# Kernel tuning notes

Measured on AMD Instinct MI355X. Metric: run time of the kernel, lower is better.

Reference implementation:

```python
import jax, jax.numpy as jnp
import numpy as np

HID = 128      # hidden_dim
CDIM = 128     # c_dim
NBLK = 5       # n_blocks
RESO = 32      # grid_resolution
G = RESO ** 3  # number of voxels
B, T = 2, 100000


def setup_inputs() -> dict:
    key = jax.random.key(0)
    ks = jax.random.split(key, 8)
    return {
        "points": jax.random.normal(ks[0], (B, T, 3), jnp.float32),
        "index": jax.random.randint(ks[1], (B, 1, T), 0, G, dtype=jnp.int64),
        # fc_pos: Linear(3, 2*HID)
        "fc_pos_w": jax.random.normal(ks[2], (3, 2 * HID), jnp.float32) * 0.1,
        "fc_pos_b": jnp.zeros((2 * HID,), jnp.float32),
        # ResnetBlockFC(2*HID, HID) x NBLK: fc_0 (2H->H), fc_1 (H->H), shortcut (2H->H, no bias)
        "fc0_w": jax.random.normal(ks[3], (NBLK, 2 * HID, HID), jnp.float32) * 0.05,
        "fc0_b": jnp.zeros((NBLK, HID), jnp.float32),
        "fc1_w": jax.random.normal(ks[4], (NBLK, HID, HID), jnp.float32) * 0.05,
        "fc1_b": jnp.zeros((NBLK, HID), jnp.float32),
        "sc_w": jax.random.normal(ks[5], (NBLK, 2 * HID, HID), jnp.float32) * 0.05,
        # fc_c: Linear(HID, CDIM)
        "fc_c_w": jax.random.normal(ks[6], (HID, CDIM), jnp.float32) * 0.05,
        "fc_c_b": jnp.zeros((CDIM,), jnp.float32),
    }


def _resnet_block(x, w0, b0, w1, b1, ws):
    # ResnetBlockFC: net = fc_0(relu(x)); dx = fc_1(relu(net)); out = shortcut(x) + dx
    net = jnp.maximum(x, 0.0) @ w0 + b0
    dx = jnp.maximum(net, 0.0) @ w1 + b1
    return x @ ws + dx


def reference(points, index, fc_pos_w, fc_pos_b, fc0_w, fc0_b, fc1_w, fc1_b, sc_w, fc_c_w, fc_c_b):
    idx = index[:, 0, :]  # [B, T]

    def pool_local(net):
        # scatter_max over voxels, then gather back per point
        seg = jax.vmap(lambda c_b, i_b: jax.ops.segment_max(c_b, i_b, num_segments=G))(net, idx)  # [B,G,H]
        return jnp.take_along_axis(seg, idx[:, :, None], axis=1)  # [B,T,H]; every gathered voxel is non-empty

    net = points @ fc_pos_w + fc_pos_b          # [B,T,2H]
    net = _resnet_block(net, fc0_w[0], fc0_b[0], fc1_w[0], fc1_b[0], sc_w[0])  # [B,T,H]
    for i in range(1, NBLK):
        pooled = pool_local(net)
        net = jnp.concatenate([net, pooled], axis=2)  # [B,T,2H]
        net = _resnet_block(net, fc0_w[i], fc0_b[i], fc1_w[i], fc1_b[i], sc_w[i])

    c = net @ fc_c_w + fc_c_b  # [B,T,CDIM]

    # generate_grid_features: scatter_mean into the 32^3 grid (zeros for empty voxels)
    sums = jax.vmap(lambda c_b, i_b: jax.ops.segment_sum(c_b, i_b, num_segments=G))(c, idx)  # [B,G,CDIM]
    cnts = jax.vmap(lambda i_b: jax.ops.segment_sum(jnp.ones((T,), c.dtype), i_b, num_segments=G))(idx)  # [B,G]
    cnts = cnts[:, :, None]
    mean = jnp.where(cnts > 0, sums / jnp.maximum(cnts, 1.0), 0.0)
    fea_grid = jnp.transpose(mean, (0, 2, 1)).reshape(B, CDIM, RESO, RESO, RESO)
    return fea_grid
```

## Files before the change

kernel.cpp:

```cpp
#include <hip/hip_runtime.h>

#define T_PTS 100000
#define NB 2
#define NROWS (NB * T_PTS)
#define GCELLS 32768
#define NCELL (NB * GCELLS)
#define HID 128
#define MBLK 64
#define GRID_RB (NROWS / MBLK)

typedef __attribute__((ext_vector_type(8))) short bf16x8;
typedef __attribute__((ext_vector_type(4))) float f32x4;

#define MFMA16 __builtin_amdgcn_mfma_f32_16x16x32_bf16

__device__ __forceinline__ unsigned short bf16rne(float f) {
  unsigned u = __float_as_uint(f);
  return (unsigned short)((u + 0x7FFFu + ((u >> 16) & 1u)) >> 16);
}
__device__ __forceinline__ void bf16split(float f, unsigned short& h,
                                          unsigned short& l) {
  h = bf16rne(f);
  l = bf16rne(f - __uint_as_float(((unsigned)h) << 16));
}
__device__ __forceinline__ unsigned packhl(float f) {
  unsigned short h, l;
  bf16split(f, h, l);
  return (((unsigned)h) << 16) | (unsigned)l;
}

union U8 { bf16x8 v; unsigned u[4]; };

__device__ __forceinline__ void up2(unsigned w0, unsigned w1, unsigned& h,
                                    unsigned& l) {
  h = __builtin_amdgcn_perm(w1, w0, 0x07060302u);
  l = __builtin_amdgcn_perm(w1, w0, 0x05040100u);
}

__device__ __forceinline__ void relu2(unsigned qh, unsigned ql, unsigned& rh,
                                      unsigned& rl) {
  const unsigned keep = ((~qh >> 15) & 0x00010001u) * 0xFFFFu;
  rh = qh & keep;
  rl = ql & keep;
}

__device__ __forceinline__ void dma16(const unsigned* g, unsigned* l) {
  __builtin_amdgcn_global_load_lds(
      (const __attribute__((address_space(1))) unsigned*)g,
      (__attribute__((address_space(3))) unsigned*)l, 16, 0, 0);
}

template <int MODE>
__global__ __launch_bounds__(256, 4) void resblock_mfma(
    const void* __restrict__ srcv, const float* __restrict__ posw,
    const float* __restrict__ posb, const unsigned* __restrict__ cell,
    const int* __restrict__ perm, const int* __restrict__ vcell,
    const unsigned short* __restrict__ w0p, const float* __restrict__ b0,
    const unsigned short* __restrict__ w1p, const float* __restrict__ b1,
    const unsigned short* __restrict__ swp, unsigned* __restrict__ net_out) {
  __shared__ unsigned lds32[8192];
  const int tid = threadIdx.x;
  const int lane = tid & 63;
  const int wid = tid >> 6;
  const int wc = wid;
  const int t0 = blockIdx.x * MBLK;

  const int srow = wid * 16 + (lane & 15);
  const int skc4 = (lane >> 4) * 4;
  const long vrow = (long)t0 + srow;
  const unsigned* nrowL = nullptr;
  const unsigned* crowL = nullptr;
  float pp0 = 0.f, pp1 = 0.f, pp2 = 0.f;
  if (MODE == 1) {
    nrowL = (const unsigned*)srcv + vrow * HID;
    crowL = cell + (long)vcell[vrow] * HID;
  } else {
    const float* ppp = (const float*)srcv + (long)perm[vrow] * 3;
    pp0 = ppp[0]; pp1 = ppp[1]; pp2 = ppp[2];
  }

  auto stage_dma = [&](int ks) {
    unsigned* base = &lds32[((ks & 1) << 11) + wid * 256];
    const unsigned* rowp = (ks < 4) ? nrowL : crowL;
    const int ko = ((ks & 3) << 4) + skc4;
    dma16(rowp + ko, base);
    dma16(rowp + 64 + ko, base + 1024);
  };
  auto stage0 = [&](int ks) {
    const int kb = ks * 32 + (lane >> 4) * 8;
    float xv[8];
#pragma unroll
    for (int i = 0; i < 8; i += 4) {
      float4 wa = *(const float4*)(posw + kb + i);
      float4 wb = *(const float4*)(posw + 256 + kb + i);
      float4 wcc = *(const float4*)(posw + 512 + kb + i);
      float4 bb = *(const float4*)(posb + kb + i);
      xv[i + 0] = fmaf(pp0, wa.x, fmaf(pp1, wb.x, fmaf(pp2, wcc.x, bb.x)));
      xv[i + 1] = fmaf(pp0, wa.y, fmaf(pp1, wb.y, fmaf(pp2, wcc.y, bb.y)));
      xv[i + 2] = fmaf(pp0, wa.z, fmaf(pp1, wb.z, fmaf(pp2, wcc.z, bb.z)));
      xv[i + 3] = fmaf(pp0, wa.w, fmaf(pp1, wb.w, fmaf(pp2, wcc.w, bb.w)));
    }
    unsigned ph[8];
#pragma unroll
    for (int i = 0; i < 8; ++i) ph[i] = packhl(xv[i]);
    uint4 xh4, xl4;
    up2(ph[0], ph[1], xh4.x, xl4.x);
    up2(ph[2], ph[3], xh4.y, xl4.y);
    up2(ph[4], ph[5], xh4.z, xl4.z);
    up2(ph[6], ph[7], xh4.w, xl4.w);
    const int db = ((ks & 1) << 11) + wid * 256 + lane * 4;
    *(uint4*)&lds32[db] = xh4;
    *(uint4*)&lds32[db + 1024] = xl4;
  };
  auto load_B = [&](const unsigned short* base, int loOff, int ks, bf16x8* h,
                    bf16x8* l) {
#pragma unroll
    for (int nt = 0; nt < 2; ++nt) {
      const int fi = (ks * 8 + wc * 2 + nt) * 512 + lane * 8;
      h[nt] = *(const bf16x8*)(base + fi);
      l[nt] = *(const bf16x8*)(base + loOff + fi);
    }
  };

  f32x4 accy[4][2], acco[4][2];
#pragma unroll
  for (int i = 0; i < 4; ++i)
#pragma unroll
    for (int j = 0; j < 2; ++j) {
      f32x4 z = {0.f, 0.f, 0.f, 0.f};
      accy[i][j] = z;
      acco[i][j] = z;
    }

  bf16x8 b1h[2], b1l[2], b2h[2], b2l[2];
  if (MODE == 1) {
    stage_dma(0);
  } else {
    stage0(0);
  }
  load_B(w0p, 32768, 0, b1h, b1l);
  __syncthreads();

#pragma unroll 1
  for (int ks = 0; ks < 8; ++ks) {
    const int sb = (ks & 1) << 11;
    load_B(swp, 32768, ks, b2h, b2l);
    if (MODE == 1 && ks < 7) stage_dma(ks + 1);
    __builtin_amdgcn_s_setprio(1);
#pragma unroll
    for (int mt = 0; mt < 4; ++mt) {
      const unsigned* px = &lds32[sb + mt * 256 + lane * 4];
      U8 xh, xl, rh, rl;
      xh.v = *(const bf16x8*)px;
      xl.v = *(const bf16x8*)(px + 1024);
#pragma unroll
      for (int i = 0; i < 4; ++i) relu2(xh.u[i], xl.u[i], rh.u[i], rl.u[i]);
#pragma unroll
      for (int nt = 0; nt < 2; ++nt) {
        accy[mt][nt] = MFMA16(rh.v, b1h[nt], accy[mt][nt], 0, 0, 0);
        accy[mt][nt] = MFMA16(rh.v, b1l[nt], accy[mt][nt], 0, 0, 0);
        accy[mt][nt] = MFMA16(rl.v, b1h[nt], accy[mt][nt], 0, 0, 0);
      }
    }
    __builtin_amdgcn_s_setprio(0);
    asm volatile("" ::: "memory");
    if (ks < 7) load_B(w0p, 32768, ks + 1, b1h, b1l);
    __builtin_amdgcn_s_setprio(1);
#pragma unroll
    for (int mt = 0; mt < 4; ++mt) {
      const unsigned* px = &lds32[sb + mt * 256 + lane * 4];
      bf16x8 xh = *(const bf16x8*)px;
      bf16x8 xl = *(const bf16x8*)(px + 1024);
#pragma unroll
      for (int nt = 0; nt < 2; ++nt) {
        acco[mt][nt] = MFMA16(xh, b2h[nt], acco[mt][nt], 0, 0, 0);
        acco[mt][nt] = MFMA16(xh, b2l[nt], acco[mt][nt], 0, 0, 0);
        acco[mt][nt] = MFMA16(xl, b2h[nt], acco[mt][nt], 0, 0, 0);
      }
    }
    __builtin_amdgcn_s_setprio(0);
    if (MODE == 0 && ks < 7) stage0(ks + 1);
    __syncthreads();
  }

  {
    float b0v[2];
#pragma unroll
    for (int nt = 0; nt < 2; ++nt)
      b0v[nt] = b0[wc * 32 + nt * 16 + (lane & 15)];
#pragma unroll
    for (int mt = 0; mt < 4; ++mt) {
#pragma unroll
      for (int nt = 0; nt < 2; ++nt) {
        const int c = wc * 32 + nt * 16 + (lane & 15);
        const int k2 = c >> 5;
        const int j = c & 7;
        const int lahi = ((c & 31) >> 3) * 16;
#pragma unroll
        for (int r = 0; r < 4; ++r) {
          float h = fmaxf(accy[mt][nt][r] + b0v[nt], 0.f);
          int la = lahi + (lane >> 4) * 4 + r;
          la ^= (la >> 3) & 7;
          lds32[((k2 * 4 + mt) * 64 + la) * 8 + j] = packhl(h);
        }
      }
    }
  }
  __syncthreads();

  {
    const int lar2 = lane ^ ((lane >> 3) & 7);
#pragma unroll
    for (int k2 = 0; k2 < 4; ++k2) {
      bf16x8 ch[2], cl[2];
      load_B(w1p, 16384, k2, ch, cl);
      __builtin_amdgcn_s_setprio(1);
#pragma unroll
      for (int mt = 0; mt < 4; ++mt) {
        const unsigned* p = &lds32[((k2 * 4 + mt) * 64 + lar2) * 8];
        uint4 q1 = *(const uint4*)p;
        uint4 q2 = *(const uint4*)(p + 4);
        unsigned q[8] = {q1.x, q1.y, q1.z, q1.w, q2.x, q2.y, q2.z, q2.w};
        U8 ah, al;
#pragma unroll
        for (int p2 = 0; p2 < 4; ++p2)
          up2(q[2 * p2], q[2 * p2 + 1], ah.u[p2], al.u[p2]);
#pragma unroll
        for (int nt = 0; nt < 2; ++nt) {
          acco[mt][nt] = MFMA16(ah.v, ch[nt], acco[mt][nt], 0, 0, 0);
          acco[mt][nt] = MFMA16(ah.v, cl[nt], acco[mt][nt], 0, 0, 0);
          acco[mt][nt] = MFMA16(al.v, ch[nt], acco[mt][nt], 0, 0, 0);
        }
      }
      __builtin_amdgcn_s_setprio(0);
    }
  }

  {
    float b1v[2];
#pragma unroll
    for (int nt = 0; nt < 2; ++nt)
      b1v[nt] = b1[wc * 32 + nt * 16 + (lane & 15)];
#pragma unroll
    for (int mt = 0; mt < 4; ++mt) {
#pragma unroll
      for (int r = 0; r < 4; ++r) {
        const int row = mt * 16 + (lane >> 4) * 4 + r;
        unsigned short* op =
            (unsigned short*)(net_out + ((long)t0 + row) * HID);
        unsigned short h, l;
        bf16split(acco[mt][0][r] + b1v[0], h, l);
        op[wc * 32 + (lane & 15)] = h;
        op[128 + wc * 32 + (lane & 15)] = l;
        bf16split(acco[mt][1][r] + b1v[1], h, l);
        op[wc * 32 + 16 + (lane & 15)] = h;
        op[128 + wc * 32 + 16 + (lane & 15)] = l;
      }
    }
  }
}

__global__ __launch_bounds__(256, 4) void final_mfma(
    unsigned* __restrict__ net, const unsigned short* __restrict__ wcp,
    const float* __restrict__ bc) {
  __shared__ unsigned lds32[4096];
  const int tid = threadIdx.x;
  const int lane = tid & 63;
  const int wid = tid >> 6;
  const int wc = wid;
  const int t0 = blockIdx.x * MBLK;

  const int srow = wid * 16 + (lane & 15);
  const int skc4 = (lane >> 4) * 4;
  const unsigned* nrowL = net + ((long)t0 + srow) * HID;

  auto stage = [&](int ks) {
    unsigned* base = &lds32[((ks & 1) << 11) + wid * 256];
    const int ko = (ks << 4) + skc4;
    dma16(nrowL + ko, base);
    dma16(nrowL + 64 + ko, base + 1024);
  };
  auto load_B = [&](int ks, bf16x8* h, bf16x8* l) {
#pragma unroll
    for (int nt = 0; nt < 2; ++nt) {
      const int fi = (ks * 8 + wc * 2 + nt) * 512 + lane * 8;
      h[nt] = *(const bf16x8*)(wcp + fi);
      l[nt] = *(const bf16x8*)(wcp + 16384 + fi);
    }
  };

  f32x4 acc[4][2];
#pragma unroll
  for (int i = 0; i < 4; ++i)
#pragma unroll
    for (int j = 0; j < 2; ++j) {
      f32x4 z = {0.f, 0.f, 0.f, 0.f};
      acc[i][j] = z;
    }

  bf16x8 ch[2], cl[2];
  stage(0);
  load_B(0, ch, cl);
  __syncthreads();

#pragma unroll 1
  for (int ks = 0; ks < 4; ++ks) {
    const int sb = (ks & 1) << 11;
    if (ks < 3) stage(ks + 1);
    __builtin_amdgcn_s_setprio(1);
#pragma unroll
    for (int mt = 0; mt < 2; ++mt) {
      const unsigned* px = &lds32[sb + mt * 256 + lane * 4];
      bf16x8 xh = *(const bf16x8*)px;
      bf16x8 xl = *(const bf16x8*)(px + 1024);
#pragma unroll
      for (int nt = 0; nt < 2; ++nt) {
        acc[mt][nt] = MFMA16(xh, ch[nt], acc[mt][nt], 0, 0, 0);
        acc[mt][nt] = MFMA16(xh, cl[nt], acc[mt][nt], 0, 0, 0);
        acc[mt][nt] = MFMA16(xl, ch[nt], acc[mt][nt], 0, 0, 0);
      }
    }
    __builtin_amdgcn_s_setprio(0);
    bf16x8 sh[2], sl[2];
#pragma unroll
    for (int nt = 0; nt < 2; ++nt) { sh[nt] = ch[nt]; sl[nt] = cl[nt]; }
    if (ks < 3) load_B(ks + 1, ch, cl);
    __builtin_amdgcn_s_setprio(1);
#pragma unroll
    for (int mt = 2; mt < 4; ++mt) {
      const unsigned* px = &lds32[sb + mt * 256 + lane * 4];
      bf16x8 xh = *(const bf16x8*)px;
      bf16x8 xl = *(const bf16x8*)(px + 1024);
#pragma unroll
      for (int nt = 0; nt < 2; ++nt) {
        acc[mt][nt] = MFMA16(xh, sh[nt], acc[mt][nt], 0, 0, 0);
        acc[mt][nt] = MFMA16(xh, sl[nt], acc[mt][nt], 0, 0, 0);
        acc[mt][nt] = MFMA16(xl, sh[nt], acc[mt][nt], 0, 0, 0);
      }
    }
    __builtin_amdgcn_s_setprio(0);
    __syncthreads();
  }

  float* fout = (float*)net;
  float bcv[2];
#pragma unroll
  for (int nt = 0; nt < 2; ++nt)
    bcv[nt] = bc[wc * 32 + nt * 16 + (lane & 15)];
#pragma unroll
  for (int mt = 0; mt < 4; ++mt) {
#pragma unroll
    for (int r = 0; r < 4; ++r) {
      const int row = mt * 16 + (lane >> 4) * 4 + r;
      float* op = fout + ((long)t0 + row) * HID;
      op[wc * 32 + (lane & 15)] = acc[mt][0][r] + bcv[0];
      op[wc * 32 + 16 + (lane & 15)] = acc[mt][1][r] + bcv[1];
    }
  }
}

__global__ void pack_weights(const float* __restrict__ fc0,
                             const float* __restrict__ fc1,
                             const float* __restrict__ sc,
                             const float* __restrict__ fcc,
                             unsigned short* __restrict__ w0p,
                             unsigned short* __restrict__ w1p,
                             unsigned short* __restrict__ swp,
                             unsigned short* __restrict__ wcp) {
  int gid = blockIdx.x * 256 + threadIdx.x;
  const float* src;
  unsigned short* dst;
  int K, e;
  if (gid < 163840) { src = fc0; dst = w0p; K = 256; e = gid; }
  else if (gid < 327680) { src = sc; dst = swp; K = 256; e = gid - 163840; }
  else if (gid < 409600) { src = fc1; dst = w1p; K = 128; e = gid - 327680; }
  else if (gid < 425984) { src = fcc; dst = wcp; K = 128; e = gid - 409600; }
  else return;
  const int mat = e / (K * 128);
  const int r = e - mat * K * 128;
  const int k = r >> 7, n = r & 127;
  const float x = src[e];
  unsigned short hi, lo;
  bf16split(x, hi, lo);
  const int ks = k >> 5, lg = (k >> 3) & 3, j = k & 7;
  const int l = lg * 16 + (n & 15), nt = n >> 4;
  unsigned short* mb = dst + (long)mat * K * 256;
  const int off = ((ks * 8 + nt) * 64 + l) * 8 + j;
  mb[off] = hi;
  mb[off + K * 128] = lo;
}

__global__ void zero_i32(int* __restrict__ p, int n) {
  const int i = blockIdx.x * 256 + threadIdx.x;
  if (i < n) p[i] = 0;
}

__global__ void count_csr(const int* __restrict__ idx, int* __restrict__ curs) {
  const int gid = blockIdx.x * 256 + threadIdx.x;
  if (gid >= NROWS) return;
  const int b = gid / T_PTS;
  atomicAdd(&curs[b * GCELLS + idx[gid]], 1);
}

__global__ __launch_bounds__(1024) void scan_csr(const int* __restrict__ cnt,
                                                 int* __restrict__ offsets) {
  __shared__ int part[1024];
  const int t = threadIdx.x;
  const int base = t * (NCELL / 1024);
  int s = 0;
  for (int i = 0; i < NCELL / 1024; ++i) s += cnt[base + i];
  part[t] = s;
  __syncthreads();
  for (int d = 1; d < 1024; d <<= 1) {
    int v = (t >= d) ? part[t - d] : 0;
    __syncthreads();
    part[t] += v;
    __syncthreads();
  }
  int run = (t == 0) ? 0 : part[t - 1];
  for (int i = 0; i < NCELL / 1024; ++i) {
    offsets[base + i] = run;
    run += cnt[base + i];
  }
  if (t == 1023) offsets[NCELL] = run;
}

__global__ void scatter_csr(const int* __restrict__ idx,
                            const int* __restrict__ offsets,
                            int* __restrict__ curs, int* __restrict__ perm,
                            int* __restrict__ vcell) {
  const int gid = blockIdx.x * 256 + threadIdx.x;
  if (gid >= NROWS) return;
  const int b = gid / T_PTS;
  const int cellk = b * GCELLS + idx[gid];
  const int slot = offsets[cellk] + atomicAdd(&curs[cellk], 1);
  perm[slot] = gid;
  vcell[slot] = cellk;
}

__global__ __launch_bounds__(256) void pool_csr(const unsigned* __restrict__ net,
                                                const int* __restrict__ offsets,
                                                unsigned* __restrict__ cellf) {
  const int cellk = blockIdx.x * 4 + (threadIdx.x >> 6);
  const int lane = threadIdx.x & 63;
  const int s0 = offsets[cellk], s1 = offsets[cellk + 1];
  if (s0 >= s1) return;
  float m0 = -3.402823466e38f, m1 = -3.402823466e38f;
  unsigned h0 = 0u, l0 = 0u, h1 = 0u, l1 = 0u;
  for (int row = s0; row < s1; ++row) {
    const unsigned* rp = net + (long)row * HID;
    unsigned hi = rp[lane];
    unsigned lo = rp[64 + lane];
    float v0 = __uint_as_float(hi << 16) + __uint_as_float(lo << 16);
    float v1 = __uint_as_float(hi & 0xFFFF0000u) +
               __uint_as_float(lo & 0xFFFF0000u);
    if (v0 > m0) { m0 = v0; h0 = hi; l0 = lo; }
    if (v1 > m1) { m1 = v1; h1 = hi; l1 = lo; }
  }
  unsigned* cp = cellf + (long)cellk * HID;
  cp[lane] = (h0 & 0xFFFFu) | (h1 & 0xFFFF0000u);
  cp[64 + lane] = (l0 & 0xFFFFu) | (l1 & 0xFFFF0000u);
}

__global__ __launch_bounds__(256) void cellsum_mean(
    const float* __restrict__ c, const int* __restrict__ offsets,
    float* __restrict__ out) {
  __shared__ float ts[64][129];
  __shared__ float cf[64];
  const int t = threadIdx.x;
  const int b = blockIdx.x >> 9;
  const int g0 = (blockIdx.x & 511) * 64;
  const int cell0 = b * GCELLS + g0;
  {
    const int ci = t >> 2;
    const int c0 = (t & 3) * 32;
    const int s0 = offsets[cell0 + ci], s1 = offsets[cell0 + ci + 1];
    float acc[32];
#pragma unroll
    for (int j = 0; j < 32; ++j) acc[j] = 0.f;
    for (int row = s0; row < s1; ++row) {
      const float* rp = c + (long)row * HID + c0;
#pragma unroll
      for (int j = 0; j < 32; j += 4) {
        float4 v = *(const float4*)(rp + j);
        acc[j + 0] += v.x;
        acc[j + 1] += v.y;
        acc[j + 2] += v.z;
        acc[j + 3] += v.w;
      }
    }
#pragma unroll
    for (int j = 0; j < 32; ++j) ts[ci][c0 + j] = acc[j];
    if ((t & 3) == 0) cf[ci] = (float)(s1 - s0);
  }
  __syncthreads();
  const int lane = t & 63;
  const int w = t >> 6;
  float* ob = out + (long)b * HID * GCELLS + g0 + lane;
  const float cnt = cf[lane];
  const bool nz = cnt > 0.f;
  const float inv = nz ? 1.0f / cnt : 0.f;
#pragma unroll 4
  for (int cc = w; cc < HID; cc += 4) {
    float v = ts[lane][cc] * inv;
    ob[(long)cc * GCELLS] = nz ? v : 0.f;
  }
}

extern "C" void kernel_launch(void* const* d_in, const int* in_sizes, int n_in,
                              void* d_out, int out_size, void* d_ws,
                              size_t ws_size, hipStream_t stream) {
  const float* points = (const float*)d_in[0];
  const int* idx = (const int*)d_in[1];
  const float* fc_pos_w = (const float*)d_in[2];
  const float* fc_pos_b = (const float*)d_in[3];
  const float* fc0_w = (const float*)d_in[4];
  const float* fc0_b = (const float*)d_in[5];
  const float* fc1_w = (const float*)d_in[6];
  const float* fc1_b = (const float*)d_in[7];
  const float* sc_w = (const float*)d_in[8];
  const float* fc_c_w = (const float*)d_in[9];
  const float* fc_c_b = (const float*)d_in[10];
  float* out = (float*)d_out;

  const long NET_BYTES = (long)NROWS * HID * 4;
  const long CELL_BYTES = (long)NCELL * HID * 4;
  unsigned* net = (unsigned*)d_ws;
  unsigned* cellf = (unsigned*)((char*)d_ws + NET_BYTES);
  int* offsets = (int*)((char*)d_ws + NET_BYTES + CELL_BYTES);

  unsigned short* packs = (unsigned short*)d_out;
  unsigned short* w0p = packs;
  unsigned short* swp = packs + 327680;
  unsigned short* w1p = packs + 655360;
  unsigned short* wcp = packs + 819200;
  int* curs = (int*)((char*)d_out + (2l << 20));
  int* perm = (int*)((char*)d_out + (3l << 20));
  int* vcell = (int*)((char*)d_out + (4l << 20));

  const int GRID_PTS = (NROWS + 255) / 256;
  const int GRID_ZERO = (NCELL + 255) / 256;
  const int GRID_CELL = NCELL / 4;
  const int GRID_CM = NCELL / 64;

  pack_weights<<<1664, 256, 0, stream>>>(fc0_w, fc1_w, sc_w, fc_c_w, w0p, w1p,
                                         swp, wcp);

  zero_i32<<<GRID_ZERO, 256, 0, stream>>>(curs, NCELL);
  count_csr<<<GRID_PTS, 256, 0, stream>>>(idx, curs);
  scan_csr<<<1, 1024, 0, stream>>>(curs, offsets);
  zero_i32<<<GRID_ZERO, 256, 0, stream>>>(curs, NCELL);
  scatter_csr<<<GRID_PTS, 256, 0, stream>>>(idx, offsets, curs, perm, vcell);

  resblock_mfma<0><<<GRID_RB, 256, 0, stream>>>(
      points, fc_pos_w, fc_pos_b, nullptr, perm, vcell, w0p, fc0_b, w1p,
      fc1_b, swp, net);

  for (int i = 1; i < 5; ++i) {
    pool_csr<<<GRID_CELL, 256, 0, stream>>>(net, offsets, cellf);
    resblock_mfma<1><<<GRID_RB, 256, 0, stream>>>(
        net, nullptr, nullptr, cellf, perm, vcell, w0p + (long)i * 65536,
        fc0_b + i * HID, w1p + (long)i * 32768, fc1_b + i * HID,
        swp + (long)i * 65536, net);
  }

  final_mfma<<<GRID_RB, 256, 0, stream>>>(net, wcp, fc_c_b);
  cellsum_mean<<<GRID_CM, 256, 0, stream>>>((const float*)net, offsets, out);
}
```

Measured before the change: 721.9 us.

## Switch resnet and final GEMMs from 16x16x32 to 32x32x16 bf16 MFMA

Replaces the 16x16x32 bf16 MFMA tiling with 32x32x16 MFMA in the resnet block and final linear kernels. Each wave now owns two 32x32 output tiles instead of eight 16x16 tiles. The packed weight layout, the LDS layout for the intermediate activation and the epilogue row/column mapping are all rewritten to match. The larger MFMA shape needs fewer instructions and fewer B-fragment loads per FLOP. In exchange it uses larger accumulators and changes the LDS access patterns, which could cause bank conflicts in the new hidden-activation store layout.

```diff
diff --git a/kernel.cpp b/kernel.cpp
--- a/kernel.cpp
+++ b/kernel.cpp
@@ -10,9 +10,9 @@
 #define GRID_RB (NROWS / MBLK)
 
 typedef __attribute__((ext_vector_type(8))) short bf16x8;
-typedef __attribute__((ext_vector_type(4))) float f32x4;
-
-#define MFMA16 __builtin_amdgcn_mfma_f32_16x16x32_bf16
+typedef __attribute__((ext_vector_type(16))) float f32x16;
+
+#define MFMA32 __builtin_amdgcn_mfma_f32_32x32x16_bf16
 
 __device__ __forceinline__ unsigned short bf16rne(float f) {
   unsigned u = __float_as_uint(f);
@@ -115,22 +115,19 @@
   auto load_B = [&](const unsigned short* base, int loOff, int ks, bf16x8* h,
                     bf16x8* l) {
 #pragma unroll
-    for (int nt = 0; nt < 2; ++nt) {
-      const int fi = (ks * 8 + wc * 2 + nt) * 512 + lane * 8;
-      h[nt] = *(const bf16x8*)(base + fi);
-      l[nt] = *(const bf16x8*)(base + loOff + fi);
+    for (int kh = 0; kh < 2; ++kh) {
+      const int fi = ((ks * 2 + kh) * 4 + wc) * 512 + lane * 8;
+      h[kh] = *(const bf16x8*)(base + fi);
+      l[kh] = *(const bf16x8*)(base + loOff + fi);
     }
   };
 
-  f32x4 accy[4][2], acco[4][2];
-#pragma unroll
-  for (int i = 0; i < 4; ++i)
-#pragma unroll
-    for (int j = 0; j < 2; ++j) {
-      f32x4 z = {0.f, 0.f, 0.f, 0.f};
-      accy[i][j] = z;
-      acco[i][j] = z;
-    }
+  f32x16 accy[2], acco[2];
+#pragma unroll
+  for (int i = 0; i < 2; ++i) {
+#pragma unroll
+    for (int j = 0; j < 16; ++j) { accy[i][j] = 0.f; acco[i][j] = 0.f; }
+  }
 
   bf16x8 b1h[2], b1l[2], b2h[2], b2l[2];
   if (MODE == 1) {
@@ -140,6 +137,10 @@
   }
   load_B(w0p, 32768, 0, b1h, b1l);
   __syncthreads();
+
+  const int amt0 = (lane >> 4) & 1;
+  const int akq0 = lane >> 5;
+  const int ari = lane & 15;
 
 #pragma unroll 1
   for (int ks = 0; ks < 8; ++ks) {
@@ -148,18 +149,19 @@
     if (MODE == 1 && ks < 7) stage_dma(ks + 1);
     __builtin_amdgcn_s_setprio(1);
 #pragma unroll
-    for (int mt = 0; mt < 4; ++mt) {
-      const unsigned* px = &lds32[sb + mt * 256 + lane * 4];
-      U8 xh, xl, rh, rl;
-      xh.v = *(const bf16x8*)px;
-      xl.v = *(const bf16x8*)(px + 1024);
-#pragma unroll
-      for (int i = 0; i < 4; ++i) relu2(xh.u[i], xl.u[i], rh.u[i], rl.u[i]);
-#pragma unroll
-      for (int nt = 0; nt < 2; ++nt) {
-        accy[mt][nt] = MFMA16(rh.v, b1h[nt], accy[mt][nt], 0, 0, 0);
-        accy[mt][nt] = MFMA16(rh.v, b1l[nt], accy[mt][nt], 0, 0, 0);
-        accy[mt][nt] = MFMA16(rl.v, b1h[nt], accy[mt][nt], 0, 0, 0);
+    for (int rt = 0; rt < 2; ++rt) {
+#pragma unroll
+      for (int kh = 0; kh < 2; ++kh) {
+        const unsigned* px = &lds32[sb + (rt * 2 + amt0) * 256 +
+                                    ((kh * 2 + akq0) * 16 + ari) * 4];
+        U8 xh, xl, rh, rl;
+        xh.v = *(const bf16x8*)px;
+        xl.v = *(const bf16x8*)(px + 1024);
+#pragma unroll
+        for (int i = 0; i < 4; ++i) relu2(xh.u[i], xl.u[i], rh.u[i], rl.u[i]);
+        accy[rt] = MFMA32(rh.v, b1h[kh], accy[rt], 0, 0, 0);
+        accy[rt] = MFMA32(rh.v, b1l[kh], accy[rt], 0, 0, 0);
+        accy[rt] = MFMA32(rl.v, b1h[kh], accy[rt], 0, 0, 0);
       }
     }
     __builtin_amdgcn_s_setprio(0);
@@ -167,15 +169,16 @@
     if (ks < 7) load_B(w0p, 32768, ks + 1, b1h, b1l);
     __builtin_amdgcn_s_setprio(1);
 #pragma unroll
-    for (int mt = 0; mt < 4; ++mt) {
-      const unsigned* px = &lds32[sb + mt * 256 + lane * 4];
-      bf16x8 xh = *(const bf16x8*)px;
-      bf16x8 xl = *(const bf16x8*)(px + 1024);
-#pragma unroll
-      for (int nt = 0; nt < 2; ++nt) {
-        acco[mt][nt] = MFMA16(xh, b2h[nt], acco[mt][nt], 0, 0, 0);
-        acco[mt][nt] = MFMA16(xh, b2l[nt], acco[mt][nt], 0, 0, 0);
-        acco[mt][nt] = MFMA16(xl, b2h[nt], acco[mt][nt], 0, 0, 0);
+    for (int rt = 0; rt < 2; ++rt) {
+#pragma unroll
+      for (int kh = 0; kh < 2; ++kh) {
+        const unsigned* px = &lds32[sb + (rt * 2 + amt0) * 256 +
+                                    ((kh * 2 + akq0) * 16 + ari) * 4];
+        bf16x8 xh = *(const bf16x8*)px;
+        bf16x8 xl = *(const bf16x8*)(px + 1024);
+        acco[rt] = MFMA32(xh, b2h[kh], acco[rt], 0, 0, 0);
+        acco[rt] = MFMA32(xh, b2l[kh], acco[rt], 0, 0, 0);
+        acco[rt] = MFMA32(xl, b2h[kh], acco[rt], 0, 0, 0);
       }
     }
     __builtin_amdgcn_s_setprio(0);
@@ -183,78 +186,66 @@
     __syncthreads();
   }
 
+  const int cCol = wc * 32 + (lane & 31);
   {
-    float b0v[2];
-#pragma unroll
-    for (int nt = 0; nt < 2; ++nt)
-      b0v[nt] = b0[wc * 32 + nt * 16 + (lane & 15)];
-#pragma unroll
-    for (int mt = 0; mt < 4; ++mt) {
-#pragma unroll
-      for (int nt = 0; nt < 2; ++nt) {
-        const int c = wc * 32 + nt * 16 + (lane & 15);
-        const int k2 = c >> 5;
-        const int j = c & 7;
-        const int lahi = ((c & 31) >> 3) * 16;
-#pragma unroll
-        for (int r = 0; r < 4; ++r) {
-          float h = fmaxf(accy[mt][nt][r] + b0v[nt], 0.f);
-          int la = lahi + (lane >> 4) * 4 + r;
-          la ^= (la >> 3) & 7;
-          lds32[((k2 * 4 + mt) * 64 + la) * 8 + j] = packhl(h);
-        }
+    const float b0v = b0[cCol];
+    const int jj = cCol & 7;
+    const int sbit = ((lane >> 3) & 1) << 5;
+    unsigned short* hb = (unsigned short*)lds32;
+#pragma unroll
+    for (int rt = 0; rt < 2; ++rt) {
+      const int f = (cCol >> 4) * 2 + rt;
+#pragma unroll
+      for (int r = 0; r < 16; ++r) {
+        const int row31 = (r & 3) + 8 * (r >> 2) + 4 * (lane >> 5);
+        float h = fmaxf(accy[rt][r] + b0v, 0.f);
+        unsigned short hh, hl;
+        bf16split(h, hh, hl);
+        const int o = (f * 64 + row31 + sbit) * 8 + jj;
+        hb[o] = hh;
+        hb[8192 + o] = hl;
       }
     }
   }
   __syncthreads();
 
   {
-    const int lar2 = lane ^ ((lane >> 3) & 7);
-#pragma unroll
-    for (int k2 = 0; k2 < 4; ++k2) {
-      bf16x8 ch[2], cl[2];
-      load_B(w1p, 16384, k2, ch, cl);
+    const unsigned short* hb = (const unsigned short*)lds32;
+#pragma unroll
+    for (int ksh2 = 0; ksh2 < 8; ++ksh2) {
+      bf16x8 ch, cl;
+      {
+        const int fi = (ksh2 * 4 + wc) * 512 + lane * 8;
+        ch = *(const bf16x8*)(w1p + fi);
+        cl = *(const bf16x8*)(w1p + 16384 + fi);
+      }
       __builtin_amdgcn_s_setprio(1);
 #pragma unroll
-      for (int mt = 0; mt < 4; ++mt) {
-        const unsigned* p = &lds32[((k2 * 4 + mt) * 64 + lar2) * 8];
-        uint4 q1 = *(const uint4*)p;
-        uint4 q2 = *(const uint4*)(p + 4);
-        unsigned q[8] = {q1.x, q1.y, q1.z, q1.w, q2.x, q2.y, q2.z, q2.w};
-        U8 ah, al;
-#pragma unroll
-        for (int p2 = 0; p2 < 4; ++p2)
-          up2(q[2 * p2], q[2 * p2 + 1], ah.u[p2], al.u[p2]);
-#pragma unroll
-        for (int nt = 0; nt < 2; ++nt) {
-          acco[mt][nt] = MFMA16(ah.v, ch[nt], acco[mt][nt], 0, 0, 0);
-          acco[mt][nt] = MFMA16(ah.v, cl[nt], acco[mt][nt], 0, 0, 0);
-          acco[mt][nt] = MFMA16(al.v, ch[nt], acco[mt][nt], 0, 0, 0);
-        }
+      for (int rt = 0; rt < 2; ++rt) {
+        const int o = ((ksh2 * 2 + rt) * 64 + lane) * 8;
+        bf16x8 ah = *(const bf16x8*)(hb + o);
+        bf16x8 al = *(const bf16x8*)(hb + 8192 + o);
+        acco[rt] = MFMA32(ah, ch, acco[rt], 0, 0, 0);
+        acco[rt] = MFMA32(ah, cl, acco[rt], 0, 0, 0);
+        acco[rt] = MFMA32(al, ch, acco[rt], 0, 0, 0);
       }
       __builtin_amdgcn_s_setprio(0);
     }
   }
 
   {
-    float b1v[2];
-#pragma unroll
-    for (int nt = 0; nt < 2; ++nt)
-      b1v[nt] = b1[wc * 32 + nt * 16 + (lane & 15)];
-#pragma unroll
-    for (int mt = 0; mt < 4; ++mt) {
-#pragma unroll
-      for (int r = 0; r < 4; ++r) {
-        const int row = mt * 16 + (lane >> 4) * 4 + r;
+    const float b1v = b1[cCol];
+#pragma unroll
+    for (int rt = 0; rt < 2; ++rt) {
+#pragma unroll
+      for (int r = 0; r < 16; ++r) {
+        const int row = rt * 32 + (r & 3) + 8 * (r >> 2) + 4 * (lane >> 5);
         unsigned short* op =
             (unsigned short*)(net_out + ((long)t0 + row) * HID);
         unsigned short h, l;
-        bf16split(acco[mt][0][r] + b1v[0], h, l);
-        op[wc * 32 + (lane & 15)] = h;
-        op[128 + wc * 32 + (lane & 15)] = l;
-        bf16split(acco[mt][1][r] + b1v[1], h, l);
-        op[wc * 32 + 16 + (lane & 15)] = h;
-        op[128 + wc * 32 + 16 + (lane & 15)] = l;
+        bf16split(acco[rt][r] + b1v, h, l);
+        op[cCol] = h;
+        op[128 + cCol] = l;
       }
     }
   }
@@ -282,26 +273,28 @@
   };
   auto load_B = [&](int ks, bf16x8* h, bf16x8* l) {
 #pragma unroll
-    for (int nt = 0; nt < 2; ++nt) {
-      const int fi = (ks * 8 + wc * 2 + nt) * 512 + lane * 8;
-      h[nt] = *(const bf16x8*)(wcp + fi);
-      l[nt] = *(const bf16x8*)(wcp + 16384 + fi);
+    for (int kh = 0; kh < 2; ++kh) {
+      const int fi = ((ks * 2 + kh) * 4 + wc) * 512 + lane * 8;
+      h[kh] = *(const bf16x8*)(wcp + fi);
+      l[kh] = *(const bf16x8*)(wcp + 16384 + fi);
     }
   };
 
-  f32x4 acc[4][2];
-#pragma unroll
-  for (int i = 0; i < 4; ++i)
-#pragma unroll
-    for (int j = 0; j < 2; ++j) {
-      f32x4 z = {0.f, 0.f, 0.f, 0.f};
-      acc[i][j] = z;
-    }
+  f32x16 acc[2];
+#pragma unroll
+  for (int i = 0; i < 2; ++i) {
+#pragma unroll
+    for (int j = 0; j < 16; ++j) acc[i][j] = 0.f;
+  }
 
   bf16x8 ch[2], cl[2];
   stage(0);
   load_B(0, ch, cl);
   __syncthreads();
+
+  const int amt0 = (lane >> 4) & 1;
+  const int akq0 = lane >> 5;
+  const int ari = lane & 15;
 
 #pragma unroll 1
   for (int ks = 0; ks < 4; ++ks) {
@@ -309,52 +302,42 @@
     if (ks < 3) stage(ks + 1);
     __builtin_amdgcn_s_setprio(1);
 #pragma unroll
-    for (int mt = 0; mt < 2; ++mt) {
-      const unsigned* px = &lds32[sb + mt * 256 + lane * 4];
-      bf16x8 xh = *(const bf16x8*)px;
-      bf16x8 xl = *(const bf16x8*)(px + 1024);
-#pragma unroll
-      for (int nt = 0; nt < 2; ++nt) {
-        acc[mt][nt] = MFMA16(xh, ch[nt], acc[mt][nt], 0, 0, 0);
-        acc[mt][nt] = MFMA16(xh, cl[nt], acc[mt][nt], 0, 0, 0);
-        acc[mt][nt] = MFMA16(xl, ch[nt], acc[mt][nt], 0, 0, 0);
-      }
+    for (int rt = 0; rt < 2; ++rt) {
+      const unsigned* px0 = &lds32[sb + (rt * 2 + amt0) * 256 +
+                                   ((0 * 2 + akq0) * 16 + ari) * 4];
+      bf16x8 xh = *(const bf16x8*)px0;
+      bf16x8 xl = *(const bf16x8*)(px0 + 1024);
+      acc[rt] = MFMA32(xh, ch[0], acc[rt], 0, 0, 0);
+      acc[rt] = MFMA32(xh, cl[0], acc[rt], 0, 0, 0);
+      acc[rt] = MFMA32(xl, ch[0], acc[rt], 0, 0, 0);
     }
     __builtin_amdgcn_s_setprio(0);
-    bf16x8 sh[2], sl[2];
-#pragma unroll
-    for (int nt = 0; nt < 2; ++nt) { sh[nt] = ch[nt]; sl[nt] = cl[nt]; }
+    bf16x8 sh = ch[1], sl = cl[1];
     if (ks < 3) load_B(ks + 1, ch, cl);
     __builtin_amdgcn_s_setprio(1);
 #pragma unroll
-    for (int mt = 2; mt < 4; ++mt) {
-      const unsigned* px = &lds32[sb + mt * 256 + lane * 4];
-      bf16x8 xh = *(const bf16x8*)px;
-      bf16x8 xl = *(const bf16x8*)(px + 1024);
-#pragma unroll
-      for (int nt = 0; nt < 2; ++nt) {
-        acc[mt][nt] = MFMA16(xh, sh[nt], acc[mt][nt], 0, 0, 0);
-        acc[mt][nt] = MFMA16(xh, sl[nt], acc[mt][nt], 0, 0, 0);
-        acc[mt][nt] = MFMA16(xl, sh[nt], acc[mt][nt], 0, 0, 0);
-      }
+    for (int rt = 0; rt < 2; ++rt) {
+      const unsigned* px1 = &lds32[sb + (rt * 2 + amt0) * 256 +
+                                   ((1 * 2 + akq0) * 16 + ari) * 4];
+      bf16x8 xh = *(const bf16x8*)px1;
+      bf16x8 xl = *(const bf16x8*)(px1 + 1024);
+      acc[rt] = MFMA32(xh, sh, acc[rt], 0, 0, 0);
+      acc[rt] = MFMA32(xh, sl, acc[rt], 0, 0, 0);
+      acc[rt] = MFMA32(xl, sh, acc[rt], 0, 0, 0);
     }
     __builtin_amdgcn_s_setprio(0);
     __syncthreads();
   }
 
   float* fout = (float*)net;
-  float bcv[2];
-#pragma unroll
-  for (int nt = 0; nt < 2; ++nt)
-    bcv[nt] = bc[wc * 32 + nt * 16 + (lane & 15)];
-#pragma unroll
-  for (int mt = 0; mt < 4; ++mt) {
-#pragma unroll
-    for (int r = 0; r < 4; ++r) {
-      const int row = mt * 16 + (lane >> 4) * 4 + r;
-      float* op = fout + ((long)t0 + row) * HID;
-      op[wc * 32 + (lane & 15)] = acc[mt][0][r] + bcv[0];
-      op[wc * 32 + 16 + (lane & 15)] = acc[mt][1][r] + bcv[1];
+  const int cCol = wc * 32 + (lane & 31);
+  const float bcv = bc[cCol];
+#pragma unroll
+  for (int rt = 0; rt < 2; ++rt) {
+#pragma unroll
+    for (int r = 0; r < 16; ++r) {
+      const int row = rt * 32 + (r & 3) + 8 * (r >> 2) + 4 * (lane >> 5);
+      fout[((long)t0 + row) * HID + cCol] = acc[rt][r] + bcv;
     }
   }
 }
@@ -382,10 +365,11 @@
   const float x = src[e];
   unsigned short hi, lo;
   bf16split(x, hi, lo);
-  const int ks = k >> 5, lg = (k >> 3) & 3, j = k & 7;
-  const int l = lg * 16 + (n & 15), nt = n >> 4;
+  const int ksh = k >> 4, nt = n >> 5;
+  const int l = (n & 31) | (((k >> 3) & 1) << 5);
+  const int j = k & 7;
   unsigned short* mb = dst + (long)mat * K * 256;
-  const int off = ((ks * 8 + nt) * 64 + l) * 8 + j;
+  const int off = ((ksh * 4 + nt) * 64 + l) * 8 + j;
   mb[off] = hi;
   mb[off + K * 128] = lo;
 }
```

Measured after the change: 774.5 us. 7.3% more time.
